# Optimization experiments

Hardware: AMD Instinct MI355X
Metric: run time of the kernel (lower is better)

Reference implementation:

```python
import jax, jax.numpy as jnp
import numpy as np

N = 10000      # nodes
E = 160000     # edges (avg degree 16)
C = 128        # channel multiplicity
D_DOWN = 64    # node_feats_down_irreps = 64x0e
R = 8          # radial edge features
AVG_NEIGH = 16.0
SQRT3 = 1.7320508075688772


def _glorot(key, shape):
    return jax.random.normal(key, shape, dtype=jnp.float32)


def setup_inputs() -> dict:
    key = jax.random.key(0)
    ks = jax.random.split(key, 16)
    mid = 2 * C  # 256: two 0e paths and two 1o paths stacked
    return {
        "node_attrs": jax.random.uniform(ks[0], (N, 10), dtype=jnp.float32),
        "node_feats": jax.random.normal(ks[1], (N, 4 * C), dtype=jnp.float32),  # 128x0e+128x1o
        "edge_attrs": jax.random.normal(ks[2], (E, 4), dtype=jnp.float32),      # 1x0e+1x1o sph harm
        "edge_feats": jax.random.normal(ks[3], (E, R), dtype=jnp.float32),
        "edge_index": jax.random.randint(ks[4], (2, E), 0, N, dtype=jnp.int32),
        "W_up0": _glorot(ks[5], (C, C)),
        "W_up1": _glorot(ks[6], (C, C)),
        "W_down": _glorot(ks[7], (C, D_DOWN)),
        "mlp_w1": _glorot(ks[8], (R + 2 * D_DOWN, 256)),
        "mlp_w2": _glorot(ks[9], (256, 256)),
        "mlp_w3": _glorot(ks[10], (256, 256)),
        "mlp_w4": _glorot(ks[11], (256, 4 * C)),   # conv_tp.weight_numel = 4 paths * 128
        "W_lin0": _glorot(ks[12], (mid, C)),
        "W_lin1": _glorot(ks[13], (mid, C)),
        "W_skip0": _glorot(ks[14], (C, C)),
        "W_skip1": _glorot(ks[15], (C, C)),
    }


def reference(node_attrs, node_feats, edge_attrs, edge_feats, edge_index,
              W_up0, W_up1, W_down, mlp_w1, mlp_w2, mlp_w3, mlp_w4,
              W_lin0, W_lin1, W_skip0, W_skip1):
    n = node_feats.shape[0]
    # split node feats into 0e scalars and 1o vectors
    x0 = node_feats[:, :C]                      # [N,128]
    x1 = node_feats[:, C:].reshape(n, C, 3)     # [N,128,3]
    inv_c = 1.0 / jnp.sqrt(jnp.float32(C))

    # skip connection: equivariant Linear node_feats -> hidden (per-irrep channel mix)
    sc0 = x0 @ (W_skip0 * inv_c)
    sc1 = jnp.einsum('nui,uv->nvi', x1, W_skip1 * inv_c)
    sc = jnp.concatenate([sc0, sc1.reshape(n, -1)], axis=-1)  # [N,512]

    # linear_up (node_feats -> edge_irreps) and linear_down (-> 64x0e)
    u0 = x0 @ (W_up0 * inv_c)
    u1 = jnp.einsum('nui,uv->nvi', x1, W_up1 * inv_c)
    down = x0 @ (W_down * inv_c)                # [N,64]

    sender, receiver = edge_index[0], edge_index[1]
    # augmented edge features: radial + down[sender] + down[receiver]
    aug = jnp.concatenate([edge_feats, down[sender], down[receiver]], axis=-1)  # [E,136]

    def dense(h, w):
        return h @ (w / jnp.sqrt(jnp.float32(w.shape[0])))

    h = jax.nn.silu(dense(aug, mlp_w1))
    h = jax.nn.silu(dense(h, mlp_w2))
    h = jax.nn.silu(dense(h, mlp_w3))
    tpw = dense(h, mlp_w4)                      # [E,512] per-edge TP weights
    w0, w1, w2, w3 = jnp.split(tpw, 4, axis=-1) # each [E,128]

    # gather sender features, split edge sph harmonics
    xs0 = u0[sender]                            # [E,128]
    xs1 = u1[sender]                            # [E,128,3]
    y0 = edge_attrs[:, :1]                      # [E,1]
    y1 = edge_attrs[:, 1:4]                     # [E,3]

    # CG tensor product, 'uvu' instructions (v=1):
    o0a = w0 * xs0 * y0                                         # 0e x 0e -> 0e
    o0b = w3 * jnp.einsum('eci,ei->ec', xs1, y1) / SQRT3        # 1o x 1o -> 0e
    o1a = w1[:, :, None] * xs0[:, :, None] * y1[:, None, :]     # 0e x 1o -> 1o
    o1b = w2[:, :, None] * xs1 * y0[:, :, None]                 # 1o x 0e -> 1o

    mji0 = jnp.concatenate([o0a, o0b], axis=1)                  # [E,256]
    mji1 = jnp.concatenate([o1a, o1b], axis=1)                  # [E,256,3]

    # scatter-sum over receivers
    m0 = jax.ops.segment_sum(mji0, receiver, num_segments=n)    # [N,256]
    m1 = jax.ops.segment_sum(mji1.reshape(mji1.shape[0], -1), receiver,
                             num_segments=n).reshape(n, 2 * C, 3)

    # final equivariant linear irreps_mid -> target, / avg_num_neighbors
    inv_m = 1.0 / jnp.sqrt(jnp.float32(2 * C))
    msg0 = m0 @ (W_lin0 * inv_m) / AVG_NEIGH                    # [N,128]
    msg1 = jnp.einsum('nui,uv->nvi', m1, W_lin1 * inv_m) / AVG_NEIGH  # [N,128,3]

    # reshape_irreps: [N, mul, (lmax+1)^2] = [N,128,4]
    message = jnp.concatenate([msg0[:, :, None], msg1], axis=-1)
    return (message, sc)
```

## Files before the change

kernel.cpp:

```cpp
#include <hip/hip_runtime.h>
#include <hip/hip_bf16.h>

#define N_NODES 10000
#define N_EDGES 160000
#define TPW_PLANE ((size_t)N_EDGES * 128)
#define EB 32
#define NB 16

typedef short v8s __attribute__((ext_vector_type(8)));
typedef float v4f __attribute__((ext_vector_type(4)));

__device__ __forceinline__ float bf2f(ushort u) {
    union { unsigned i; float f; } x; x.i = ((unsigned)u) << 16; return x.f;
}
__device__ __forceinline__ float fin(float x) {
    return (x == x) ? fminf(fmaxf(x, -1e30f), 1e30f) : 0.f;
}
__device__ __forceinline__ ushort f2bf(float f) {
    union { unsigned i; float f; } x; x.f = fin(f);
    unsigned i = x.i;
    unsigned r = (i + 0x7fffu + ((i >> 16) & 1u)) >> 16;
    return (ushort)r;
}
__device__ __forceinline__ unsigned cvt_pk_bf16(float lo, float hi) {
    unsigned r;
    asm("v_cvt_pk_bf16_f32 %0, %1, %2" : "=v"(r) : "v"(lo), "v"(hi));
    return r;
}
__device__ __forceinline__ float fast_rcp(float x) {
    float r;
    asm("v_rcp_f32 %0, %1" : "=v"(r) : "v"(x));
    return r;
}
__device__ __forceinline__ float silu(float x) {
    return x * fast_rcp(1.f + __expf(-x));
}

#define INV_C 0.08838834764831845f
#define S_MLP1 0.08574929257125442f
#define S_MLP 0.0625f
#define INV_SQRT3 0.5773502691896258f
#define OUT_SCALE 0.00390625f

#define MFMA __builtin_amdgcn_mfma_f32_16x16x32_bf16

__global__ __launch_bounds__(256) void pack_kernel(
    const float* __restrict__ w1, const float* __restrict__ w2,
    const float* __restrict__ w3, const float* __restrict__ w4,
    const float* __restrict__ wl0, const float* __restrict__ wl1,
    ushort* __restrict__ w1p, ushort* __restrict__ w2p,
    ushort* __restrict__ w3p, ushort* __restrict__ w4p,
    ushort* __restrict__ wl0p, ushort* __restrict__ wl1p)
{
    int idx = blockIdx.x * 256 + threadIdx.x;
    const float* W; ushort* D; int KT, Kreal, Nn, id, koff = 0;
    if (idx < 40960)       { W = w1;  D = w1p;  KT = 5; Kreal = 136; Nn = 256; id = idx; }
    else if (idx < 106496) { W = w2;  D = w2p;  KT = 8; Kreal = 256; Nn = 256; id = idx - 40960; }
    else if (idx < 172032) { W = w3;  D = w3p;  KT = 8; Kreal = 256; Nn = 256; id = idx - 106496; }
    else if (idx < 303104) { W = w4;  D = w4p;  KT = 8; Kreal = 256; Nn = 512; id = idx - 172032; }
    else if (idx < 335872) { W = wl0; D = wl0p; KT = 8; Kreal = 256; Nn = 128; id = idx - 303104; }
    else if (idx < 352256) { W = wl1; D = wl1p;         KT = 4; Kreal = 128; Nn = 128; id = idx - 335872; }
    else                   { W = wl1; D = wl1p + 16384; KT = 4; Kreal = 128; Nn = 128; id = idx - 352256; koff = 128; }
    int j = id & 7, lane = (id >> 3) & 63, tt = id >> 9;
    int kt = tt % KT, nt = tt / KT;
    int k = kt * 32 + ((lane >> 4) << 3) + j;
    int nn = nt * 16 + (lane & 15);
    D[id] = (k < Kreal) ? f2bf(W[(k + koff) * Nn + nn]) : (ushort)0;
}

__global__ __launch_bounds__(256) void node_uud_kernel(
    const float* __restrict__ nf,
    const float* __restrict__ Wu0, const float* __restrict__ Wu1,
    const float* __restrict__ Wd,
    ushort* __restrict__ u0, ushort* __restrict__ u1,
    ushort* __restrict__ down)
{
    __shared__ float x[NB * 512];
    int t = threadIdx.x;
    int n0 = blockIdx.x * NB;
    {
        const float4* src = (const float4*)(nf + (size_t)n0 * 512);
        float4* dst = (float4*)x;
        for (int i = t; i < NB * 128; i += 256) dst[i] = src[i];
    }
    __syncthreads();
    int v = t & 127, g = t >> 7;
    {
        float acc[8] = {0.f,0.f,0.f,0.f,0.f,0.f,0.f,0.f};
        for (int u = 0; u < 128; ++u) {
            float wv = Wu0[u * 128 + v];
#pragma unroll
            for (int j = 0; j < 8; ++j) acc[j] += x[(g * 8 + j) * 512 + u] * wv;
        }
#pragma unroll
        for (int j = 0; j < 8; ++j)
            u0[(size_t)(n0 + g * 8 + j) * 128 + v] = f2bf(acc[j] * INV_C);
    }
    for (int i = 0; i < 3; ++i) {
        float acc[8] = {0.f,0.f,0.f,0.f,0.f,0.f,0.f,0.f};
        for (int u = 0; u < 128; ++u) {
            float wv = Wu1[u * 128 + v];
#pragma unroll
            for (int j = 0; j < 8; ++j)
                acc[j] += x[(g * 8 + j) * 512 + 128 + u * 3 + i] * wv;
        }
#pragma unroll
        for (int j = 0; j < 8; ++j)
            u1[(size_t)(n0 + g * 8 + j) * 384 + i * 128 + v] = f2bf(acc[j] * INV_C);
    }
    {
        int vd = t & 63, gd = t >> 6;
        float acc[4] = {0.f,0.f,0.f,0.f};
        for (int u = 0; u < 128; ++u) {
            float wv = Wd[u * 64 + vd];
#pragma unroll
            for (int j = 0; j < 4; ++j) acc[j] += x[(gd * 4 + j) * 512 + u] * wv;
        }
#pragma unroll
        for (int j = 0; j < 4; ++j)
            down[(size_t)(n0 + gd * 4 + j) * 64 + vd] = f2bf(acc[j] * INV_C);
    }
}

__global__ __launch_bounds__(256) void node_sc_kernel(
    const float* __restrict__ nf,
    const float* __restrict__ Ws0, const float* __restrict__ Ws1,
    float* __restrict__ out_sc)
{
    __shared__ float x[NB * 512];
    __shared__ float xs[NB * 384];
    int t = threadIdx.x;
    int n0 = blockIdx.x * NB;
    {
        const float4* src = (const float4*)(nf + (size_t)n0 * 512);
        float4* dst = (float4*)x;
        for (int i = t; i < NB * 128; i += 256) dst[i] = src[i];
    }
    __syncthreads();
    int v = t & 127, g = t >> 7;
    {
        float acc[8] = {0.f,0.f,0.f,0.f,0.f,0.f,0.f,0.f};
        for (int u = 0; u < 128; ++u) {
            float wv = Ws0[u * 128 + v];
#pragma unroll
            for (int j = 0; j < 8; ++j) acc[j] += x[(g * 8 + j) * 512 + u] * wv;
        }
#pragma unroll
        for (int j = 0; j < 8; ++j)
            out_sc[(size_t)(n0 + g * 8 + j) * 512 + v] = fin(acc[j] * INV_C);
    }
    for (int i = 0; i < 3; ++i) {
        float acc[8] = {0.f,0.f,0.f,0.f,0.f,0.f,0.f,0.f};
        for (int u = 0; u < 128; ++u) {
            float wv = Ws1[u * 128 + v];
#pragma unroll
            for (int j = 0; j < 8; ++j)
                acc[j] += x[(g * 8 + j) * 512 + 128 + u * 3 + i] * wv;
        }
#pragma unroll
        for (int j = 0; j < 8; ++j)
            xs[(g * 8 + j) * 384 + v * 3 + i] = fin(acc[j] * INV_C);
    }
    __syncthreads();
    for (int i = t; i < NB * 96; i += 256) {
        int nd = i / 96, k = i - nd * 96;
        *(float4*)&out_sc[(size_t)(n0 + nd) * 512 + 128 + k * 4] =
            *(const float4*)&xs[nd * 384 + k * 4];
    }
}

__global__ __launch_bounds__(256) void hist_kernel(const int* __restrict__ eidx, int* __restrict__ counts)
{
    int e = blockIdx.x * 256 + threadIdx.x;
    int r = eidx[N_EDGES + e];
    if (r < 0) r = 0; if (r >= N_NODES) r = N_NODES - 1;
    atomicAdd(&counts[r], 1);
}

__global__ __launch_bounds__(1024) void scan_kernel(const int* __restrict__ counts, int* __restrict__ offs)
{
    __shared__ int buf[1024];
    __shared__ int base_s;
    int t = threadIdx.x;
    if (t == 0) { base_s = 0; offs[0] = 0; }
    __syncthreads();
    for (int chunk = 0; chunk < (N_NODES + 1023) / 1024; ++chunk) {
        int i = chunk * 1024 + t;
        int vv = (i < N_NODES) ? counts[i] : 0;
        buf[t] = vv;
        __syncthreads();
        for (int off = 1; off < 1024; off <<= 1) {
            int xv = (t >= off) ? buf[t - off] : 0;
            __syncthreads();
            buf[t] += xv;
            __syncthreads();
        }
        int incl = buf[t];
        int base = base_s;
        __syncthreads();
        if (i < N_NODES) offs[i + 1] = base + incl;
        if (t == 1023) base_s = base + incl;
        __syncthreads();
    }
}

__global__ __launch_bounds__(256) void fill_kernel(
    const int* __restrict__ eidx, const int* __restrict__ offs,
    int* __restrict__ cnt2, int* __restrict__ esort)
{
    int e = blockIdx.x * 256 + threadIdx.x;
    int r = eidx[N_EDGES + e];
    if (r < 0) r = 0; if (r >= N_NODES) r = N_NODES - 1;
    int k = atomicAdd(&cnt2[r], 1);
    int pos = offs[r] + k;
    if (pos < 0) pos = 0; if (pos >= N_EDGES) pos = N_EDGES - 1;
    esort[pos] = e;
}

#define H_STRIDE 264

template <int KT, bool SILU>
__device__ __forceinline__ void gemm_layer(
    const ushort* __restrict__ wpack, const ushort* srcLDS, int srcStride,
    ushort* dstLDS, float scale)
{
    int t = threadIdx.x;
    int w = t >> 6, l = t & 63;
    int lrow = l & 15, q = l >> 4;

    for (int p = 0; p < 2; ++p) {
        int nt0 = w * 4 + 2 * p, nt1 = nt0 + 1;
        v4f a00 = {0.f,0.f,0.f,0.f}, a01 = {0.f,0.f,0.f,0.f};
        v4f a10 = {0.f,0.f,0.f,0.f}, a11 = {0.f,0.f,0.f,0.f};
#pragma unroll
        for (int kt = 0; kt < KT; ++kt) {
            v8s b0 = *(const v8s*)&wpack[(size_t)(nt0 * KT + kt) * 512 + l * 8];
            v8s b1 = *(const v8s*)&wpack[(size_t)(nt1 * KT + kt) * 512 + l * 8];
            v8s x0 = *(const v8s*)&srcLDS[lrow * srcStride + kt * 32 + q * 8];
            v8s x1 = *(const v8s*)&srcLDS[(16 + lrow) * srcStride + kt * 32 + q * 8];
            a00 = MFMA(x0, b0, a00, 0, 0, 0);
            a01 = MFMA(x0, b1, a01, 0, 0, 0);
            a10 = MFMA(x1, b0, a10, 0, 0, 0);
            a11 = MFMA(x1, b1, a11, 0, 0, 0);
        }
#pragma unroll
        for (int r = 0; r < 4; ++r) {
            float x00 = a00[r] * scale, x01 = a01[r] * scale;
            float x10 = a10[r] * scale, x11 = a11[r] * scale;
            if (SILU) {
                x00 = silu(x00); x01 = silu(x01);
                x10 = silu(x10); x11 = silu(x11);
            }
            int row0 = q * 4 + r, row1 = row0 + 16;
            unsigned p0 = cvt_pk_bf16(x00, x01);
            dstLDS[row0 * H_STRIDE + nt0 * 16 + lrow] = (ushort)p0;
            dstLDS[row0 * H_STRIDE + nt1 * 16 + lrow] = (ushort)(p0 >> 16);
            unsigned p1 = cvt_pk_bf16(x10, x11);
            dstLDS[row1 * H_STRIDE + nt0 * 16 + lrow] = (ushort)p1;
            dstLDS[row1 * H_STRIDE + nt1 * 16 + lrow] = (ushort)(p1 >> 16);
        }
    }
    __syncthreads();
}

template <bool ATOMIC>
__device__ __forceinline__ void gemm_out(
    const ushort* __restrict__ wpack, const ushort* srcLDS,
    const int* s_rcv, float* __restrict__ out, ushort* __restrict__ tpw,
    int e0, int cofs)
{
    int t = threadIdx.x;
    int w = t >> 6, l = t & 63;
    int lrow = l & 15, q = l >> 4;
    ushort* plane = tpw + (size_t)cofs * TPW_PLANE;
    int nt0 = w * 2, nt1 = nt0 + 1;
    v4f a00 = {0.f,0.f,0.f,0.f}, a01 = {0.f,0.f,0.f,0.f};
    v4f a10 = {0.f,0.f,0.f,0.f}, a11 = {0.f,0.f,0.f,0.f};
#pragma unroll
    for (int kt = 0; kt < 8; ++kt) {
        v8s b0 = *(const v8s*)&wpack[(size_t)(nt0 * 8 + kt) * 512 + l * 8];
        v8s b1 = *(const v8s*)&wpack[(size_t)(nt1 * 8 + kt) * 512 + l * 8];
        v8s x0 = *(const v8s*)&srcLDS[lrow * H_STRIDE + kt * 32 + q * 8];
        v8s x1 = *(const v8s*)&srcLDS[(16 + lrow) * H_STRIDE + kt * 32 + q * 8];
        a00 = MFMA(x0, b0, a00, 0, 0, 0);
        a01 = MFMA(x0, b1, a01, 0, 0, 0);
        a10 = MFMA(x1, b0, a10, 0, 0, 0);
        a11 = MFMA(x1, b1, a11, 0, 0, 0);
    }
    int col0 = nt0 * 16 + lrow, col1 = col0 + 16;
#pragma unroll
    for (int r = 0; r < 4; ++r) {
        int row0 = q * 4 + r, row1 = row0 + 16;
        if constexpr (ATOMIC) {
            int rcv0 = s_rcv[row0], rcv1 = s_rcv[row1];
            atomicAdd(&out[(size_t)rcv0 * 512 + col0 * 4 + cofs], fin(a00[r] * OUT_SCALE));
            atomicAdd(&out[(size_t)rcv0 * 512 + col1 * 4 + cofs], fin(a01[r] * OUT_SCALE));
            atomicAdd(&out[(size_t)rcv1 * 512 + col0 * 4 + cofs], fin(a10[r] * OUT_SCALE));
            atomicAdd(&out[(size_t)rcv1 * 512 + col1 * 4 + cofs], fin(a11[r] * OUT_SCALE));
        } else {
            size_t base0 = (size_t)(e0 + row0) * 128;
            unsigned p0 = cvt_pk_bf16(a00[r] * OUT_SCALE, a01[r] * OUT_SCALE);
            plane[base0 + col0] = (ushort)p0;
            plane[base0 + col1] = (ushort)(p0 >> 16);
            size_t base1 = (size_t)(e0 + row1) * 128;
            unsigned p1 = cvt_pk_bf16(a10[r] * OUT_SCALE, a11[r] * OUT_SCALE);
            plane[base1 + col0] = (ushort)p1;
            plane[base1 + col1] = (ushort)(p1 >> 16);
        }
    }
}

template <bool ATOMIC>
__global__ __launch_bounds__(256, 3) void edge_msg_kernel(
    const int* __restrict__ eidx, const int* __restrict__ esort,
    const float* __restrict__ ef, const float* __restrict__ ea,
    const ushort* __restrict__ down,
    const ushort* __restrict__ u0, const ushort* __restrict__ u1,
    const ushort* __restrict__ w1p, const ushort* __restrict__ w2p,
    const ushort* __restrict__ w3p, const ushort* __restrict__ w4p,
    const ushort* __restrict__ wl0p, const ushort* __restrict__ wl1p,
    float* __restrict__ out_msg, ushort* __restrict__ tpw)
{
    __shared__ __align__(16) ushort s_hA[EB * H_STRIDE];
    __shared__ __align__(16) ushort s_hB[EB * H_STRIDE];
    __shared__ __align__(16) ushort s_q[EB * H_STRIDE];
    __shared__ int s_snd[EB];
    __shared__ int s_rcv[EB];
    __shared__ int s_eid[EB];
    __shared__ float s_y[EB][4];

    int t = threadIdx.x;
    int e0 = blockIdx.x * EB;

    if (t < EB) {
        int e;
        if constexpr (ATOMIC) {
            e = e0 + t;
        } else {
            e = esort[e0 + t];
            if (e < 0) e = 0; if (e >= N_EDGES) e = N_EDGES - 1;
        }
        s_eid[t] = e;
        int s = eidx[e];
        int r = eidx[N_EDGES + e];
        if (s < 0) s = 0; if (s >= N_NODES) s = N_NODES - 1;
        if (r < 0) r = 0; if (r >= N_NODES) r = N_NODES - 1;
        s_snd[t] = s; s_rcv[t] = r;
        s_y[t][0] = fin(ea[(size_t)e * 4 + 0]);
        s_y[t][1] = fin(ea[(size_t)e * 4 + 1]);
        s_y[t][2] = fin(ea[(size_t)e * 4 + 2]);
        s_y[t][3] = fin(ea[(size_t)e * 4 + 3]);
    }
    __syncthreads();
    {
        int e = t >> 3, c0 = (t & 7) * 21;
        int snd = s_snd[e], rcv = s_rcv[e], eid = s_eid[e];
#pragma unroll
        for (int j = 0; j < 21; ++j) {
            int cc = c0 + j;
            ushort vv;
            if (cc < 8)        vv = f2bf(ef[(size_t)eid * 8 + cc]);
            else if (cc < 72)  vv = down[(size_t)snd * 64 + (cc - 8)];
            else if (cc < 136) vv = down[(size_t)rcv * 64 + (cc - 72)];
            else               vv = 0;
            s_hB[e * 168 + cc] = vv;
        }
    }
    __syncthreads();
    gemm_layer<5, true>(w1p, s_hB, 168, s_hA, S_MLP1);
    gemm_layer<8, true>(w2p, s_hA, H_STRIDE, s_hB, S_MLP);
    gemm_layer<8, true>(w3p, s_hB, H_STRIDE, s_hA, S_MLP);

    int w = t >> 6, l = t & 63;
    int lrow = l & 15, q = l >> 4;
    int colg0 = w * 32 + lrow, colg1 = colg0 + 16;

    for (int qd = 0; qd < 4; ++qd) {
        int nt0 = qd * 8 + w * 2, nt1 = nt0 + 1;
        v4f a00 = {0.f,0.f,0.f,0.f}, a01 = {0.f,0.f,0.f,0.f};
        v4f a10 = {0.f,0.f,0.f,0.f}, a11 = {0.f,0.f,0.f,0.f};
#pragma unroll
        for (int kt = 0; kt < 8; ++kt) {
            v8s b0 = *(const v8s*)&w4p[(size_t)(nt0 * 8 + kt) * 512 + l * 8];
            v8s b1 = *(const v8s*)&w4p[(size_t)(nt1 * 8 + kt) * 512 + l * 8];
            v8s x0 = *(const v8s*)&s_hA[lrow * H_STRIDE + kt * 32 + q * 8];
            v8s x1 = *(const v8s*)&s_hA[(16 + lrow) * H_STRIDE + kt * 32 + q * 8];
            a00 = MFMA(x0, b0, a00, 0, 0, 0);
            a01 = MFMA(x0, b1, a01, 0, 0, 0);
            a10 = MFMA(x1, b0, a10, 0, 0, 0);
            a11 = MFMA(x1, b1, a11, 0, 0, 0);
        }
#pragma unroll
        for (int r = 0; r < 4; ++r) {
#pragma unroll
            for (int m = 0; m < 2; ++m) {
                int row = m * 16 + q * 4 + r;
                float v0 = (m == 0 ? a00[r] : a10[r]) * S_MLP;
                float v1 = (m == 0 ? a01[r] : a11[r]) * S_MLP;
                int snd = s_snd[row];
                if (qd == 0) {
                    float y0 = s_y[row][0];
                    float ua = bf2f(u0[(size_t)snd * 128 + colg0]);
                    float ub = bf2f(u0[(size_t)snd * 128 + colg1]);
                    unsigned pk = cvt_pk_bf16(v0 * ua * y0, v1 * ub * y0);
                    s_hB[row * H_STRIDE + colg0] = (ushort)pk;
                    s_hB[row * H_STRIDE + colg1] = (ushort)(pk >> 16);
                } else if (qd == 1) {
                    float ua = bf2f(u0[(size_t)snd * 128 + colg0]);
                    float ub = bf2f(u0[(size_t)snd * 128 + colg1]);
                    unsigned pk = cvt_pk_bf16(v0 * ua, v1 * ub);
                    s_q[row * H_STRIDE + colg0] = (ushort)pk;
                    s_q[row * H_STRIDE + colg1] = (ushort)(pk >> 16);
                } else if (qd == 2) {
                    unsigned pk = cvt_pk_bf16(v0, v1);
                    s_q[row * H_STRIDE + 128 + colg0] = (ushort)pk;
                    s_q[row * H_STRIDE + 128 + colg1] = (ushort)(pk >> 16);
                } else {
                    size_t ub_ = (size_t)snd * 384;
                    float d0 = bf2f(u1[ub_ + colg0])       * s_y[row][1]
                             + bf2f(u1[ub_ + 128 + colg0]) * s_y[row][2]
                             + bf2f(u1[ub_ + 256 + colg0]) * s_y[row][3];
                    float d1 = bf2f(u1[ub_ + colg1])       * s_y[row][1]
                             + bf2f(u1[ub_ + 128 + colg1]) * s_y[row][2]
                             + bf2f(u1[ub_ + 256 + colg1]) * s_y[row][3];
                    unsigned pk = cvt_pk_bf16(v0 * d0 * INV_SQRT3, v1 * d1 * INV_SQRT3);
                    s_hB[row * H_STRIDE + 128 + colg0] = (ushort)pk;
                    s_hB[row * H_STRIDE + 128 + colg1] = (ushort)(pk >> 16);
                }
            }
        }
    }
    __syncthreads();

    gemm_out<ATOMIC>(wl0p, s_hB, s_rcv, out_msg, tpw, e0, 0);
    __syncthreads();

    const ushort* wl1t = wl1p;
    const ushort* wl1b = wl1p + 16384;
    int ntz0 = w * 2, ntz1 = ntz0 + 1;
    int colz0 = ntz0 * 16 + lrow, colz1 = colz0 + 16;

    v4f z00 = {0.f,0.f,0.f,0.f}, z01 = {0.f,0.f,0.f,0.f};
    v4f z10 = {0.f,0.f,0.f,0.f}, z11 = {0.f,0.f,0.f,0.f};
#pragma unroll
    for (int kt = 0; kt < 4; ++kt) {
        v8s b0 = *(const v8s*)&wl1t[(size_t)(ntz0 * 4 + kt) * 512 + l * 8];
        v8s b1 = *(const v8s*)&wl1t[(size_t)(ntz1 * 4 + kt) * 512 + l * 8];
        v8s x0 = *(const v8s*)&s_q[lrow * H_STRIDE + kt * 32 + q * 8];
        v8s x1 = *(const v8s*)&s_q[(16 + lrow) * H_STRIDE + kt * 32 + q * 8];
        z00 = MFMA(x0, b0, z00, 0, 0, 0);
        z01 = MFMA(x0, b1, z01, 0, 0, 0);
        z10 = MFMA(x1, b0, z10, 0, 0, 0);
        z11 = MFMA(x1, b1, z11, 0, 0, 0);
    }

    for (int i = 0; i < 3; ++i) {
#pragma unroll
        for (int it = 0; it < 8; ++it) {
            int idx = t + it * 256;
            int e = idx >> 6, kp = (idx & 63) << 1;
            unsigned uq = *(const unsigned*)&s_q[e * H_STRIDE + 128 + kp];
            unsigned uu = *(const unsigned*)&u1[(size_t)s_snd[e] * 384 + i * 128 + kp];
            float y0 = s_y[e][0];
            float lo = bf2f((ushort)uq) * bf2f((ushort)uu) * y0;
            float hi = bf2f((ushort)(uq >> 16)) * bf2f((ushort)(uu >> 16)) * y0;
            *(unsigned*)&s_hB[e * H_STRIDE + kp] = cvt_pk_bf16(lo, hi);
        }
        __syncthreads();
        v4f p00 = {0.f,0.f,0.f,0.f}, p01 = {0.f,0.f,0.f,0.f};
        v4f p10 = {0.f,0.f,0.f,0.f}, p11 = {0.f,0.f,0.f,0.f};
#pragma unroll
        for (int kt = 0; kt < 4; ++kt) {
            v8s b0 = *(const v8s*)&wl1b[(size_t)(ntz0 * 4 + kt) * 512 + l * 8];
            v8s b1 = *(const v8s*)&wl1b[(size_t)(ntz1 * 4 + kt) * 512 + l * 8];
            v8s x0 = *(const v8s*)&s_hB[lrow * H_STRIDE + kt * 32 + q * 8];
            v8s x1 = *(const v8s*)&s_hB[(16 + lrow) * H_STRIDE + kt * 32 + q * 8];
            p00 = MFMA(x0, b0, p00, 0, 0, 0);
            p01 = MFMA(x0, b1, p01, 0, 0, 0);
            p10 = MFMA(x1, b0, p10, 0, 0, 0);
            p11 = MFMA(x1, b1, p11, 0, 0, 0);
        }
        ushort* plane = tpw + (size_t)(1 + i) * TPW_PLANE;
#pragma unroll
        for (int r = 0; r < 4; ++r) {
            int row0 = q * 4 + r, row1 = row0 + 16;
            float yi0 = s_y[row0][1 + i], yi1 = s_y[row1][1 + i];
            float v00 = (yi0 * z00[r] + p00[r]) * OUT_SCALE;
            float v01 = (yi0 * z01[r] + p01[r]) * OUT_SCALE;
            float v10 = (yi1 * z10[r] + p10[r]) * OUT_SCALE;
            float v11 = (yi1 * z11[r] + p11[r]) * OUT_SCALE;
            if constexpr (ATOMIC) {
                int rcv0 = s_rcv[row0], rcv1 = s_rcv[row1];
                atomicAdd(&out_msg[(size_t)rcv0 * 512 + colz0 * 4 + 1 + i], fin(v00));
                atomicAdd(&out_msg[(size_t)rcv0 * 512 + colz1 * 4 + 1 + i], fin(v01));
                atomicAdd(&out_msg[(size_t)rcv1 * 512 + colz0 * 4 + 1 + i], fin(v10));
                atomicAdd(&out_msg[(size_t)rcv1 * 512 + colz1 * 4 + 1 + i], fin(v11));
            } else {
                size_t base0 = (size_t)(e0 + row0) * 128;
                unsigned pk0 = cvt_pk_bf16(v00, v01);
                plane[base0 + colz0] = (ushort)pk0;
                plane[base0 + colz1] = (ushort)(pk0 >> 16);
                size_t base1 = (size_t)(e0 + row1) * 128;
                unsigned pk1 = cvt_pk_bf16(v10, v11);
                plane[base1 + colz0] = (ushort)pk1;
                plane[base1 + colz1] = (ushort)(pk1 >> 16);
            }
        }
        __syncthreads();
    }
}

__global__ __launch_bounds__(256) void gather_kernel(
    const int* __restrict__ offs,
    const ushort* __restrict__ tpw, float* __restrict__ out_msg)
{
    int n = blockIdx.x, t = threadIdx.x;
    int beg = offs[n];
    if (beg < 0) beg = 0; if (beg > N_EDGES) beg = N_EDGES;
    int end = offs[n + 1];
    if (end < beg) end = beg; if (end > N_EDGES) end = N_EDGES;
    int c = t & 63;
    int p = t >> 6;
    const unsigned* src = (const unsigned*)(tpw + (size_t)p * TPW_PLANE) + c;
    float a0 = 0.f, a1 = 0.f;
    for (int j = beg; j < end; ++j) {
        unsigned v = src[(size_t)j * 64];
        a0 += bf2f((ushort)v);
        a1 += bf2f((ushort)(v >> 16));
    }
    out_msg[(size_t)n * 512 + (2 * c) * 4 + p] = fin(a0);
    out_msg[(size_t)n * 512 + (2 * c + 1) * 4 + p] = fin(a1);
}

extern "C" void kernel_launch(void* const* d_in, const int* in_sizes, int n_in,
                              void* d_out, int out_size, void* d_ws, size_t ws_size,
                              hipStream_t stream)
{
    const float* node_feats = (const float*)d_in[1];
    const float* edge_attrs = (const float*)d_in[2];
    const float* edge_feats = (const float*)d_in[3];
    const int*   edge_index = (const int*)d_in[4];
    const float* W_up0  = (const float*)d_in[5];
    const float* W_up1  = (const float*)d_in[6];
    const float* W_down = (const float*)d_in[7];
    const float* mlp_w1 = (const float*)d_in[8];
    const float* mlp_w2 = (const float*)d_in[9];
    const float* mlp_w3 = (const float*)d_in[10];
    const float* mlp_w4 = (const float*)d_in[11];
    const float* W_lin0 = (const float*)d_in[12];
    const float* W_lin1 = (const float*)d_in[13];
    const float* W_skip0 = (const float*)d_in[14];
    const float* W_skip1 = (const float*)d_in[15];

    char* S = (char*)d_out + 20480000;

    ushort* u0    = (ushort*)(S + 0);
    ushort* down  = (ushort*)(S + 2560000);
    ushort* u1    = (ushort*)(S + 3840000);
    ushort* w1p   = (ushort*)(S + 11520000);
    ushort* w2p   = (ushort*)(S + 11601920);
    ushort* w3p   = (ushort*)(S + 11732992);
    ushort* w4p   = (ushort*)(S + 11864064);
    ushort* wl0p  = (ushort*)(S + 12126208);
    ushort* wl1p  = (ushort*)(S + 12191744);
    int*    offs  = (int*)(S + 12257280);
    int*    esort = (int*)(S + 12297312);
    int*    counts= (int*)(S + 12937312);
    int*    cnt2  = (int*)(S + 12977312);

    float* out_msg = (float*)d_out;
    float* out_sc  = (float*)d_out + (size_t)N_NODES * 512;

    const size_t TPW_BYTES = (size_t)N_EDGES * 512 * 2;
    bool bigws = (ws_size >= TPW_BYTES) && (d_ws != nullptr);
    ushort* tpw = (ushort*)d_ws;

    pack_kernel<<<1440, 256, 0, stream>>>(mlp_w1, mlp_w2, mlp_w3, mlp_w4, W_lin0, W_lin1,
                                          w1p, w2p, w3p, w4p, wl0p, wl1p);
    node_uud_kernel<<<N_NODES / NB, 256, 0, stream>>>(node_feats, W_up0, W_up1, W_down, u0, u1, down);

    if (bigws) {
        hipMemsetAsync(counts, 0, 80000, stream);
        hist_kernel<<<N_EDGES / 256, 256, 0, stream>>>(edge_index, counts);
        scan_kernel<<<1, 1024, 0, stream>>>(counts, offs);
        fill_kernel<<<N_EDGES / 256, 256, 0, stream>>>(edge_index, offs, cnt2, esort);
        edge_msg_kernel<false><<<N_EDGES / EB, 256, 0, stream>>>(edge_index, esort,
            edge_feats, edge_attrs,
            down, u0, u1, w1p, w2p, w3p, w4p, wl0p, wl1p, out_msg, tpw);
        gather_kernel<<<N_NODES, 256, 0, stream>>>(offs, tpw, out_msg);
    } else {
        hipMemsetAsync(out_msg, 0, 20480000, stream);
        edge_msg_kernel<true><<<N_EDGES / EB, 256, 0, stream>>>(edge_index, esort,
            edge_feats, edge_attrs,
            down, u0, u1, w1p, w2p, w3p, w4p, wl0p, wl1p, out_msg, tpw);
    }
    node_sc_kernel<<<N_NODES / NB, 256, 0, stream>>>(node_feats, W_skip0, W_skip1, out_sc);
}
```

Baseline: 601.2 us.

## Replace bf16 edge-message buffer plus gather with in-block segmented reduction and atomics

Removes the per-edge bf16 staging buffer and the separate gather kernel. Each edge block now writes its output tile into shared memory, sums runs of equal receivers (edges are sorted by receiver), and atomically adds the partial sums into the zeroed fp32 output. This cuts the large intermediate write and read and drops one launch, at the cost of extra syncs and atomics for receivers that span block boundaries. The change also fuses the three-component loops in the node linear kernels, reuses shared memory in node_sc, and rewrites the scan with wave shuffles.

```diff
diff --git a/kernel.cpp b/kernel.cpp
--- a/kernel.cpp
+++ b/kernel.cpp
@@ -3,7 +3,6 @@
 
 #define N_NODES 10000
 #define N_EDGES 160000
-#define TPW_PLANE ((size_t)N_EDGES * 128)
 #define EB 32
 #define NB 16
 
@@ -96,17 +95,23 @@
         for (int j = 0; j < 8; ++j)
             u0[(size_t)(n0 + g * 8 + j) * 128 + v] = f2bf(acc[j] * INV_C);
     }
-    for (int i = 0; i < 3; ++i) {
-        float acc[8] = {0.f,0.f,0.f,0.f,0.f,0.f,0.f,0.f};
+    {
+        float acc[3][8] = {};
         for (int u = 0; u < 128; ++u) {
             float wv = Wu1[u * 128 + v];
 #pragma unroll
+            for (int j = 0; j < 8; ++j) {
+                int b = (g * 8 + j) * 512 + 128 + u * 3;
+                acc[0][j] += x[b + 0] * wv;
+                acc[1][j] += x[b + 1] * wv;
+                acc[2][j] += x[b + 2] * wv;
+            }
+        }
+#pragma unroll
+        for (int i = 0; i < 3; ++i)
+#pragma unroll
             for (int j = 0; j < 8; ++j)
-                acc[j] += x[(g * 8 + j) * 512 + 128 + u * 3 + i] * wv;
-        }
-#pragma unroll
-        for (int j = 0; j < 8; ++j)
-            u1[(size_t)(n0 + g * 8 + j) * 384 + i * 128 + v] = f2bf(acc[j] * INV_C);
+                u1[(size_t)(n0 + g * 8 + j) * 384 + i * 128 + v] = f2bf(acc[i][j] * INV_C);
     }
     {
         int vd = t & 63, gd = t >> 6;
@@ -128,7 +133,6 @@
     float* __restrict__ out_sc)
 {
     __shared__ float x[NB * 512];
-    __shared__ float xs[NB * 384];
     int t = threadIdx.x;
     int n0 = blockIdx.x * NB;
     {
@@ -149,23 +153,28 @@
         for (int j = 0; j < 8; ++j)
             out_sc[(size_t)(n0 + g * 8 + j) * 512 + v] = fin(acc[j] * INV_C);
     }
-    for (int i = 0; i < 3; ++i) {
-        float acc[8] = {0.f,0.f,0.f,0.f,0.f,0.f,0.f,0.f};
-        for (int u = 0; u < 128; ++u) {
-            float wv = Ws1[u * 128 + v];
-#pragma unroll
-            for (int j = 0; j < 8; ++j)
-                acc[j] += x[(g * 8 + j) * 512 + 128 + u * 3 + i] * wv;
-        }
+    float acc[3][8] = {};
+    for (int u = 0; u < 128; ++u) {
+        float wv = Ws1[u * 128 + v];
+#pragma unroll
+        for (int j = 0; j < 8; ++j) {
+            int b = (g * 8 + j) * 512 + 128 + u * 3;
+            acc[0][j] += x[b + 0] * wv;
+            acc[1][j] += x[b + 1] * wv;
+            acc[2][j] += x[b + 2] * wv;
+        }
+    }
+    __syncthreads();
+#pragma unroll
+    for (int i = 0; i < 3; ++i)
 #pragma unroll
         for (int j = 0; j < 8; ++j)
-            xs[(g * 8 + j) * 384 + v * 3 + i] = fin(acc[j] * INV_C);
-    }
+            x[(g * 8 + j) * 384 + v * 3 + i] = fin(acc[i][j] * INV_C);
     __syncthreads();
     for (int i = t; i < NB * 96; i += 256) {
         int nd = i / 96, k = i - nd * 96;
         *(float4*)&out_sc[(size_t)(n0 + nd) * 512 + 128 + k * 4] =
-            *(const float4*)&xs[nd * 384 + k * 4];
+            *(const float4*)&x[nd * 384 + k * 4];
     }
 }
 
@@ -179,23 +188,33 @@
 
 __global__ __launch_bounds__(1024) void scan_kernel(const int* __restrict__ counts, int* __restrict__ offs)
 {
-    __shared__ int buf[1024];
+    __shared__ int wsum[16];
     __shared__ int base_s;
-    int t = threadIdx.x;
+    int t = threadIdx.x, lane = t & 63, wid = t >> 6;
     if (t == 0) { base_s = 0; offs[0] = 0; }
     __syncthreads();
     for (int chunk = 0; chunk < (N_NODES + 1023) / 1024; ++chunk) {
         int i = chunk * 1024 + t;
-        int vv = (i < N_NODES) ? counts[i] : 0;
-        buf[t] = vv;
-        __syncthreads();
-        for (int off = 1; off < 1024; off <<= 1) {
-            int xv = (t >= off) ? buf[t - off] : 0;
-            __syncthreads();
-            buf[t] += xv;
-            __syncthreads();
-        }
-        int incl = buf[t];
+        int v = (i < N_NODES) ? counts[i] : 0;
+#pragma unroll
+        for (int off = 1; off < 64; off <<= 1) {
+            int u = __shfl_up(v, off, 64);
+            if (lane >= off) v += u;
+        }
+        if (lane == 63) wsum[wid] = v;
+        __syncthreads();
+        if (wid == 0) {
+            int s = (lane < 16) ? wsum[lane] : 0;
+#pragma unroll
+            for (int off = 1; off < 16; off <<= 1) {
+                int u = __shfl_up(s, off, 64);
+                if (lane >= off) s += u;
+            }
+            if (lane < 16) wsum[lane] = s;
+        }
+        __syncthreads();
+        int prefix = (wid > 0) ? wsum[wid - 1] : 0;
+        int incl = v + prefix;
         int base = base_s;
         __syncthreads();
         if (i < N_NODES) offs[i + 1] = base + incl;
@@ -263,16 +282,32 @@
     __syncthreads();
 }
 
-template <bool ATOMIC>
+__device__ __forceinline__ void reduce_plane(
+    const float* s_red, const int* s_rcv, float* __restrict__ out_msg, int cofs)
+{
+    int t = threadIdx.x;
+    int c = t & 127, h = t >> 7;
+    float sum = 0.f;
+    int cur = s_rcv[h * 16];
+#pragma unroll
+    for (int row = h * 16; row < h * 16 + 16; ++row) {
+        int rcv = s_rcv[row];
+        if (rcv != cur) {
+            atomicAdd(&out_msg[(size_t)cur * 512 + c * 4 + cofs], sum);
+            sum = 0.f; cur = rcv;
+        }
+        sum += s_red[row * 128 + c];
+    }
+    atomicAdd(&out_msg[(size_t)cur * 512 + c * 4 + cofs], sum);
+}
+
 __device__ __forceinline__ void gemm_out(
     const ushort* __restrict__ wpack, const ushort* srcLDS,
-    const int* s_rcv, float* __restrict__ out, ushort* __restrict__ tpw,
-    int e0, int cofs)
+    const int* s_rcv, float* __restrict__ out_msg, float* s_red, int cofs)
 {
     int t = threadIdx.x;
     int w = t >> 6, l = t & 63;
     int lrow = l & 15, q = l >> 4;
-    ushort* plane = tpw + (size_t)cofs * TPW_PLANE;
     int nt0 = w * 2, nt1 = nt0 + 1;
     v4f a00 = {0.f,0.f,0.f,0.f}, a01 = {0.f,0.f,0.f,0.f};
     v4f a10 = {0.f,0.f,0.f,0.f}, a11 = {0.f,0.f,0.f,0.f};
@@ -291,26 +326,15 @@
 #pragma unroll
     for (int r = 0; r < 4; ++r) {
         int row0 = q * 4 + r, row1 = row0 + 16;
-        if constexpr (ATOMIC) {
-            int rcv0 = s_rcv[row0], rcv1 = s_rcv[row1];
-            atomicAdd(&out[(size_t)rcv0 * 512 + col0 * 4 + cofs], fin(a00[r] * OUT_SCALE));
-            atomicAdd(&out[(size_t)rcv0 * 512 + col1 * 4 + cofs], fin(a01[r] * OUT_SCALE));
-            atomicAdd(&out[(size_t)rcv1 * 512 + col0 * 4 + cofs], fin(a10[r] * OUT_SCALE));
-            atomicAdd(&out[(size_t)rcv1 * 512 + col1 * 4 + cofs], fin(a11[r] * OUT_SCALE));
-        } else {
-            size_t base0 = (size_t)(e0 + row0) * 128;
-            unsigned p0 = cvt_pk_bf16(a00[r] * OUT_SCALE, a01[r] * OUT_SCALE);
-            plane[base0 + col0] = (ushort)p0;
-            plane[base0 + col1] = (ushort)(p0 >> 16);
-            size_t base1 = (size_t)(e0 + row1) * 128;
-            unsigned p1 = cvt_pk_bf16(a10[r] * OUT_SCALE, a11[r] * OUT_SCALE);
-            plane[base1 + col0] = (ushort)p1;
-            plane[base1 + col1] = (ushort)(p1 >> 16);
-        }
-    }
-}
-
-template <bool ATOMIC>
+        s_red[row0 * 128 + col0] = a00[r] * OUT_SCALE;
+        s_red[row0 * 128 + col1] = a01[r] * OUT_SCALE;
+        s_red[row1 * 128 + col0] = a10[r] * OUT_SCALE;
+        s_red[row1 * 128 + col1] = a11[r] * OUT_SCALE;
+    }
+    __syncthreads();
+    reduce_plane(s_red, s_rcv, out_msg, cofs);
+}
+
 __global__ __launch_bounds__(256, 3) void edge_msg_kernel(
     const int* __restrict__ eidx, const int* __restrict__ esort,
     const float* __restrict__ ef, const float* __restrict__ ea,
@@ -319,7 +343,7 @@
     const ushort* __restrict__ w1p, const ushort* __restrict__ w2p,
     const ushort* __restrict__ w3p, const ushort* __restrict__ w4p,
     const ushort* __restrict__ wl0p, const ushort* __restrict__ wl1p,
-    float* __restrict__ out_msg, ushort* __restrict__ tpw)
+    float* __restrict__ out_msg)
 {
     __shared__ __align__(16) ushort s_hA[EB * H_STRIDE];
     __shared__ __align__(16) ushort s_hB[EB * H_STRIDE];
@@ -329,17 +353,14 @@
     __shared__ int s_eid[EB];
     __shared__ float s_y[EB][4];
 
+    float* s_red = (float*)s_hA;
+
     int t = threadIdx.x;
     int e0 = blockIdx.x * EB;
 
     if (t < EB) {
-        int e;
-        if constexpr (ATOMIC) {
-            e = e0 + t;
-        } else {
-            e = esort[e0 + t];
-            if (e < 0) e = 0; if (e >= N_EDGES) e = N_EDGES - 1;
-        }
+        int e = esort[e0 + t];
+        if (e < 0) e = 0; if (e >= N_EDGES) e = N_EDGES - 1;
         s_eid[t] = e;
         int s = eidx[e];
         int r = eidx[N_EDGES + e];
@@ -432,13 +453,12 @@
     }
     __syncthreads();
 
-    gemm_out<ATOMIC>(wl0p, s_hB, s_rcv, out_msg, tpw, e0, 0);
+    gemm_out(wl0p, s_hB, s_rcv, out_msg, s_red, 0);
     __syncthreads();
 
     const ushort* wl1t = wl1p;
     const ushort* wl1b = wl1p + 16384;
     int ntz0 = w * 2, ntz1 = ntz0 + 1;
-    int colz0 = ntz0 * 16 + lrow, colz1 = colz0 + 16;
 
     v4f z00 = {0.f,0.f,0.f,0.f}, z01 = {0.f,0.f,0.f,0.f};
     v4f z10 = {0.f,0.f,0.f,0.f}, z11 = {0.f,0.f,0.f,0.f};
@@ -454,6 +474,7 @@
         z11 = MFMA(x1, b1, z11, 0, 0, 0);
     }
 
+    int colz0 = ntz0 * 16 + lrow, colz1 = colz0 + 16;
     for (int i = 0; i < 3; ++i) {
 #pragma unroll
         for (int it = 0; it < 8; ++it) {
@@ -480,56 +501,19 @@
             p10 = MFMA(x1, b0, p10, 0, 0, 0);
             p11 = MFMA(x1, b1, p11, 0, 0, 0);
         }
-        ushort* plane = tpw + (size_t)(1 + i) * TPW_PLANE;
 #pragma unroll
         for (int r = 0; r < 4; ++r) {
             int row0 = q * 4 + r, row1 = row0 + 16;
             float yi0 = s_y[row0][1 + i], yi1 = s_y[row1][1 + i];
-            float v00 = (yi0 * z00[r] + p00[r]) * OUT_SCALE;
-            float v01 = (yi0 * z01[r] + p01[r]) * OUT_SCALE;
-            float v10 = (yi1 * z10[r] + p10[r]) * OUT_SCALE;
-            float v11 = (yi1 * z11[r] + p11[r]) * OUT_SCALE;
-            if constexpr (ATOMIC) {
-                int rcv0 = s_rcv[row0], rcv1 = s_rcv[row1];
-                atomicAdd(&out_msg[(size_t)rcv0 * 512 + colz0 * 4 + 1 + i], fin(v00));
-                atomicAdd(&out_msg[(size_t)rcv0 * 512 + colz1 * 4 + 1 + i], fin(v01));
-                atomicAdd(&out_msg[(size_t)rcv1 * 512 + colz0 * 4 + 1 + i], fin(v10));
-                atomicAdd(&out_msg[(size_t)rcv1 * 512 + colz1 * 4 + 1 + i], fin(v11));
-            } else {
-                size_t base0 = (size_t)(e0 + row0) * 128;
-                unsigned pk0 = cvt_pk_bf16(v00, v01);
-                plane[base0 + colz0] = (ushort)pk0;
-                plane[base0 + colz1] = (ushort)(pk0 >> 16);
-                size_t base1 = (size_t)(e0 + row1) * 128;
-                unsigned pk1 = cvt_pk_bf16(v10, v11);
-                plane[base1 + colz0] = (ushort)pk1;
-                plane[base1 + colz1] = (ushort)(pk1 >> 16);
-            }
-        }
-        __syncthreads();
-    }
-}
-
-__global__ __launch_bounds__(256) void gather_kernel(
-    const int* __restrict__ offs,
-    const ushort* __restrict__ tpw, float* __restrict__ out_msg)
-{
-    int n = blockIdx.x, t = threadIdx.x;
-    int beg = offs[n];
-    if (beg < 0) beg = 0; if (beg > N_EDGES) beg = N_EDGES;
-    int end = offs[n + 1];
-    if (end < beg) end = beg; if (end > N_EDGES) end = N_EDGES;
-    int c = t & 63;
-    int p = t >> 6;
-    const unsigned* src = (const unsigned*)(tpw + (size_t)p * TPW_PLANE) + c;
-    float a0 = 0.f, a1 = 0.f;
-    for (int j = beg; j < end; ++j) {
-        unsigned v = src[(size_t)j * 64];
-        a0 += bf2f((ushort)v);
-        a1 += bf2f((ushort)(v >> 16));
-    }
-    out_msg[(size_t)n * 512 + (2 * c) * 4 + p] = fin(a0);
-    out_msg[(size_t)n * 512 + (2 * c + 1) * 4 + p] = fin(a1);
+            s_red[row0 * 128 + colz0] = (yi0 * z00[r] + p00[r]) * OUT_SCALE;
+            s_red[row0 * 128 + colz1] = (yi0 * z01[r] + p01[r]) * OUT_SCALE;
+            s_red[row1 * 128 + colz0] = (yi1 * z10[r] + p10[r]) * OUT_SCALE;
+            s_red[row1 * 128 + colz1] = (yi1 * z11[r] + p11[r]) * OUT_SCALE;
+        }
+        __syncthreads();
+        reduce_plane(s_red, s_rcv, out_msg, 1 + i);
+        __syncthreads();
+    }
 }
 
 extern "C" void kernel_launch(void* const* d_in, const int* in_sizes, int n_in,
@@ -571,28 +555,19 @@
     float* out_msg = (float*)d_out;
     float* out_sc  = (float*)d_out + (size_t)N_NODES * 512;
 
-    const size_t TPW_BYTES = (size_t)N_EDGES * 512 * 2;
-    bool bigws = (ws_size >= TPW_BYTES) && (d_ws != nullptr);
-    ushort* tpw = (ushort*)d_ws;
-
     pack_kernel<<<1440, 256, 0, stream>>>(mlp_w1, mlp_w2, mlp_w3, mlp_w4, W_lin0, W_lin1,
                                           w1p, w2p, w3p, w4p, wl0p, wl1p);
     node_uud_kernel<<<N_NODES / NB, 256, 0, stream>>>(node_feats, W_up0, W_up1, W_down, u0, u1, down);
 
-    if (bigws) {
-        hipMemsetAsync(counts, 0, 80000, stream);
-        hist_kernel<<<N_EDGES / 256, 256, 0, stream>>>(edge_index, counts);
-        scan_kernel<<<1, 1024, 0, stream>>>(counts, offs);
-        fill_kernel<<<N_EDGES / 256, 256, 0, stream>>>(edge_index, offs, cnt2, esort);
-        edge_msg_kernel<false><<<N_EDGES / EB, 256, 0, stream>>>(edge_index, esort,
-            edge_feats, edge_attrs,
-            down, u0, u1, w1p, w2p, w3p, w4p, wl0p, wl1p, out_msg, tpw);
-        gather_kernel<<<N_NODES, 256, 0, stream>>>(offs, tpw, out_msg);
-    } else {
-        hipMemsetAsync(out_msg, 0, 20480000, stream);
-        edge_msg_kernel<true><<<N_EDGES / EB, 256, 0, stream>>>(edge_index, esort,
-            edge_feats, edge_attrs,
-            down, u0, u1, w1p, w2p, w3p, w4p, wl0p, wl1p, out_msg, tpw);
-    }
+    hipMemsetAsync(counts, 0, 80000, stream);
+    hipMemsetAsync(out_msg, 0, 20480000, stream);
+    hist_kernel<<<N_EDGES / 256, 256, 0, stream>>>(edge_index, counts);
+    scan_kernel<<<1, 1024, 0, stream>>>(counts, offs);
+    fill_kernel<<<N_EDGES / 256, 256, 0, stream>>>(edge_index, offs, cnt2, esort);
+
+    edge_msg_kernel<<<N_EDGES / EB, 256, 0, stream>>>(edge_index, esort,
+        edge_feats, edge_attrs,
+        down, u0, u1, w1p, w2p, w3p, w4p, wl0p, wl1p, out_msg);
+
     node_sc_kernel<<<N_NODES / NB, 256, 0, stream>>>(node_feats, W_skip0, W_skip1, out_sc);
 }
```

Result: faster. 552.1 us (-8.2%).
